# Optimization experiments

Measured on AMD Instinct MI355X. Metric: run time of the kernel, lower is better.

The kernel has to match this reference:

```python
import jax, jax.numpy as jnp
import numpy as np

NUM_EXPERTS = 8
TOP_K = 2
N_EMBD = 1024
B, T = 4, 2048


def setup_inputs() -> dict:
    key = jax.random.key(0)
    k_x, k_g, k_e = jax.random.split(key, 3)
    x = jax.random.normal(k_x, (B, T, N_EMBD), dtype=jnp.float32)
    # torch nn.Linear weight layout: (out_features, in_features); y = x @ W.T
    scale = 1.0 / np.sqrt(N_EMBD)
    gate_w = jax.random.uniform(k_g, (NUM_EXPERTS, N_EMBD), dtype=jnp.float32,
                                minval=-scale, maxval=scale)
    expert_w = jax.random.uniform(k_e, (NUM_EXPERTS, N_EMBD, N_EMBD), dtype=jnp.float32,
                                  minval=-scale, maxval=scale)
    return {"x": x, "gate_w": gate_w, "expert_w": expert_w}


def reference(x, gate_w, expert_w):
    Bb, Tt, C = x.shape
    xf = x.reshape(Bb * Tt, C)                        # (N, C)
    logits = xf @ gate_w.T                            # (N, E)
    w, sel = jax.lax.top_k(logits, TOP_K)             # (N, K) each
    # softmax over the selected logits in float32, cast back (matches torch)
    w = jax.nn.softmax(w.astype(jnp.float32), axis=1).astype(xf.dtype)
    # scatter per-token routing weights into a dense (N, E) combine matrix
    n = xf.shape[0]
    w_full = jnp.zeros((n, NUM_EXPERTS), dtype=xf.dtype)
    w_full = w_full.at[jnp.arange(n)[:, None], sel].add(w)
    # all-expert outputs: y_e = x @ W_e.T  -> (N, E, C)
    expert_out = jnp.einsum('nc,edc->ned', xf, expert_w)
    out = jnp.einsum('ne,ned->nd', w_full, expert_out)  # combine
    return out.reshape(Bb, Tt, C)
```

## Files before the change

### kernel.cpp

```cpp
#include <hip/hip_runtime.h>
#include <hip/hip_bf16.h>

#define NEXP 8
#define NEMB 1024
#define NTOK 8192
#define BM 128
#define BN 256
#define BK 64
#define NK  (NEMB / BK)
#define RBSLOTS 20
#define BLD_STRIPE 512

typedef __attribute__((ext_vector_type(8))) short  bf16x8;
typedef __attribute__((ext_vector_type(8))) unsigned short u16x8;
typedef __attribute__((ext_vector_type(4))) float  f32x4;

#define XB_BYTES   (NTOK * NEMB * 2)
#define WB_BYTES   (NEXP * NEMB * NEMB * 2)
#define CNT_OFF    (XB_BYTES + WB_BYTES)
#define LTOK_OFF   (CNT_OFF + 256)
#define LWT_OFF    (LTOK_OFF + NEXP * NTOK * 4)
#define SELW_OFF   (LWT_OFF + NEXP * NTOK * 4)

__device__ __forceinline__ unsigned short f2bf(float f) {
    unsigned u = __builtin_bit_cast(unsigned, f);
    unsigned r = (u + 0x7fffu + ((u >> 16) & 1u)) >> 16;
    return (unsigned short)r;
}

__global__ void k_cvt_w(const float* __restrict__ w, unsigned short* __restrict__ wb) {
    int i = (blockIdx.x * blockDim.x + threadIdx.x) * 8;
    f32x4 v0 = *reinterpret_cast<const f32x4*>(w + i);
    f32x4 v1 = *reinterpret_cast<const f32x4*>(w + i + 4);
    u16x8 o;
#pragma unroll
    for (int j = 0; j < 4; ++j) { o[j] = f2bf(v0[j]); o[4 + j] = f2bf(v1[j]); }
    *reinterpret_cast<u16x8*>(wb + i) = o;
}

__global__ __launch_bounds__(256)
void k_gate(const float* __restrict__ x, const float* __restrict__ gw,
            unsigned short* __restrict__ xb, int4* __restrict__ selw) {
    int t = threadIdx.x, wave = t >> 6, lane = t & 63;
    int n = blockIdx.x * 4 + wave;

    const float* xr = x + (size_t)n * NEMB + lane * 16;
    f32x4 xv[4];
#pragma unroll
    for (int j = 0; j < 4; ++j) xv[j] = *reinterpret_cast<const f32x4*>(xr + j * 4);

    u16x8 o0, o1;
#pragma unroll
    for (int q = 0; q < 4; ++q) {
        o0[q] = f2bf(xv[0][q]); o0[4 + q] = f2bf(xv[1][q]);
        o1[q] = f2bf(xv[2][q]); o1[4 + q] = f2bf(xv[3][q]);
    }
    u16x8* xo = reinterpret_cast<u16x8*>(xb + (size_t)n * NEMB + lane * 16);
    xo[0] = o0; xo[1] = o1;

    float p[NEXP];
#pragma unroll
    for (int e = 0; e < NEXP; ++e) {
        const float* gr = gw + e * NEMB + lane * 16;
        f32x4 a = xv[0] * *reinterpret_cast<const f32x4*>(gr);
#pragma unroll
        for (int j = 1; j < 4; ++j) a += xv[j] * *reinterpret_cast<const f32x4*>(gr + j * 4);
        p[e] = a[0] + a[1] + a[2] + a[3];
    }
#pragma unroll
    for (int e = 0; e < NEXP; ++e) {
        float v = p[e];
#pragma unroll
        for (int m = 1; m < 64; m <<= 1) v += __shfl_xor(v, m, 64);
        p[e] = v;
    }
    if (lane == 0) {
        int e0 = 0; float b0 = p[0];
#pragma unroll
        for (int e = 1; e < NEXP; ++e) if (p[e] > b0) { b0 = p[e]; e0 = e; }
        int e1 = -1; float b1 = -3.4e38f;
#pragma unroll
        for (int e = 0; e < NEXP; ++e) if (e != e0 && p[e] > b1) { b1 = p[e]; e1 = e; }
        float ex = __expf(b1 - b0);
        float inv = 1.f / (1.f + ex);
        int4 s;
        s.x = e0; s.y = e1;
        s.z = __float_as_int(inv); s.w = __float_as_int(ex * inv);
        selw[n] = s;
    }
}

__global__ __launch_bounds__(256)
void k_build(const int4* __restrict__ selw, int* __restrict__ counts,
             int* __restrict__ ltok, float* __restrict__ lwt) {
    int e = blockIdx.y;
    int n0 = blockIdx.x * BLD_STRIPE;
    __shared__ int lcnt, base;
    __shared__ int   toks[BLD_STRIPE];
    __shared__ float wts[BLD_STRIPE];
    if (threadIdx.x == 0) lcnt = 0;
    __syncthreads();
    for (int i = threadIdx.x; i < BLD_STRIPE; i += 256) {
        int4 s = selw[n0 + i];
        if (s.x == e) {
            int p = atomicAdd(&lcnt, 1);
            toks[p] = n0 + i; wts[p] = __int_as_float(s.z);
        }
        if (s.y == e) {
            int p = atomicAdd(&lcnt, 1);
            toks[p] = n0 + i; wts[p] = __int_as_float(s.w);
        }
    }
    __syncthreads();
    if (threadIdx.x == 0) base = atomicAdd(&counts[e], lcnt);
    __syncthreads();
    for (int i = threadIdx.x; i < lcnt; i += 256) {
        ltok[e * NTOK + base + i] = toks[i];
        lwt[e * NTOK + base + i]  = wts[i];
    }
}

__global__ void k_pad(const int* __restrict__ counts, int* __restrict__ ltok,
                      float* __restrict__ lwt) {
    int e = blockIdx.x;
    int c = counts[e];
    int cp = (c + BM - 1) & ~(BM - 1);
    for (int i = c + threadIdx.x; i < cp; i += blockDim.x) {
        ltok[e * NTOK + i] = -1;
        lwt[e * NTOK + i]  = 0.f;
    }
}

__global__ __launch_bounds__(512, 2)
void k_gemm(const unsigned short* __restrict__ xb, const unsigned short* __restrict__ wb,
            const int* __restrict__ counts, const int* __restrict__ ltok,
            const float* __restrict__ lwt, float* __restrict__ out) {
    int e  = blockIdx.z;
    int rb = blockIdx.y;
    int cb = blockIdx.x;
    int cnt = counts[e];
    if (rb * BM >= cnt) return;

    __shared__ unsigned short As[3][BM * BK];
    __shared__ unsigned short Bs[3][BN * BK];
    __shared__ int   tokS[BM];
    __shared__ float wS[BM];

    int t = threadIdx.x;
    int lane = t & 63, wave = t >> 6;
    int wr = wave >> 2, wc = wave & 3;

    if (t < BM) {
        tokS[t] = ltok[e * NTOK + rb * BM + t];
        wS[t]   = lwt[e * NTOK + rb * BM + t];
    }

    const unsigned short* aSrc[2]; int aOff[2];
    const unsigned short* bSrc[4]; int bOff[4];
#pragma unroll
    for (int i = 0; i < 2; ++i) {
        int idx = i * 512 + t;
        int r   = idx >> 3;
        int csw = (idx & 7) ^ (r & 7);
        int tok = ltok[e * NTOK + rb * BM + r];
        int tokc = tok < 0 ? 0 : tok;
        aSrc[i] = xb + (size_t)tokc * NEMB + csw * 8;
        aOff[i] = (i * 512 + wave * 64) * 8;
    }
#pragma unroll
    for (int i = 0; i < 4; ++i) {
        int idx = i * 512 + t;
        int r   = idx >> 3;
        int csw = (idx & 7) ^ (r & 7);
        bSrc[i] = wb + (size_t)e * NEMB * NEMB + (size_t)(cb * BN + r) * NEMB + csw * 8;
        bOff[i] = (i * 512 + wave * 64) * 8;
    }

#define STAGE(aDst, bDst, kk)                                                       \
    {                                                                               \
        _Pragma("unroll")                                                           \
        for (int i = 0; i < 2; ++i)                                                 \
            __builtin_amdgcn_global_load_lds(                                       \
                (const __attribute__((address_space(1))) void*)(aSrc[i] + (kk) * BK),\
                (__attribute__((address_space(3))) void*)((aDst) + aOff[i]), 16, 0, 0);\
        _Pragma("unroll")                                                           \
        for (int i = 0; i < 4; ++i)                                                 \
            __builtin_amdgcn_global_load_lds(                                       \
                (const __attribute__((address_space(1))) void*)(bSrc[i] + (kk) * BK),\
                (__attribute__((address_space(3))) void*)((bDst) + bOff[i]), 16, 0, 0);\
    }

    f32x4 acc[4][4];
#pragma unroll
    for (int m = 0; m < 4; ++m)
#pragma unroll
        for (int n = 0; n < 4; ++n) acc[m][n] = (f32x4){0.f, 0.f, 0.f, 0.f};

    int fr = lane & 15, fq = lane >> 4, fs = fr & 7;

#define COMPUTE(aRd, bRd)                                                           \
    {                                                                               \
        _Pragma("unroll")                                                           \
        for (int ks = 0; ks < 2; ++ks) {                                            \
            int ch = (fq + 4 * ks) ^ fs;                                            \
            bf16x8 af[4], bfr[4];                                                   \
            _Pragma("unroll")                                                       \
            for (int m = 0; m < 4; ++m)                                             \
                af[m] = *reinterpret_cast<const bf16x8*>(                           \
                    (aRd) + (wr * 64 + m * 16 + fr) * BK + ch * 8);                 \
            _Pragma("unroll")                                                       \
            for (int n = 0; n < 4; ++n)                                             \
                bfr[n] = *reinterpret_cast<const bf16x8*>(                          \
                    (bRd) + (wc * 64 + n * 16 + fr) * BK + ch * 8);                 \
            __builtin_amdgcn_s_setprio(1);                                          \
            _Pragma("unroll")                                                       \
            for (int m = 0; m < 4; ++m)                                             \
                _Pragma("unroll")                                                   \
                for (int n = 0; n < 4; ++n)                                         \
                    acc[m][n] = __builtin_amdgcn_mfma_f32_16x16x32_bf16(            \
                        af[m], bfr[n], acc[m][n], 0, 0, 0);                         \
            __builtin_amdgcn_s_setprio(0);                                          \
        }                                                                           \
    }

    unsigned short *aRd = &As[0][0], *aMid = &As[1][0], *aWr = &As[2][0];
    unsigned short *bRd = &Bs[0][0], *bMid = &Bs[1][0], *bWr = &Bs[2][0];

    STAGE(aRd, bRd, 0);
    STAGE(aMid, bMid, 1);

    for (int kt = 0; kt < NK - 2; ++kt) {
        asm volatile("s_waitcnt vmcnt(6)" ::: "memory");
        __builtin_amdgcn_s_barrier();
        STAGE(aWr, bWr, kt + 2);
        COMPUTE(aRd, bRd);
        asm volatile("s_waitcnt lgkmcnt(0)" ::: "memory");
        __builtin_amdgcn_s_barrier();
        unsigned short* tmp;
        tmp = aRd; aRd = aMid; aMid = aWr; aWr = tmp;
        tmp = bRd; bRd = bMid; bMid = bWr; bWr = tmp;
    }
    asm volatile("s_waitcnt vmcnt(6)" ::: "memory");
    __builtin_amdgcn_s_barrier();
    COMPUTE(aRd, bRd);
    asm volatile("s_waitcnt lgkmcnt(0)" ::: "memory");
    __builtin_amdgcn_s_barrier();
    {
        unsigned short* tmp;
        tmp = aRd; aRd = aMid; aMid = aWr; aWr = tmp;
        tmp = bRd; bRd = bMid; bMid = bWr; bWr = tmp;
    }
    asm volatile("s_waitcnt vmcnt(0)" ::: "memory");
    __builtin_amdgcn_s_barrier();
    COMPUTE(aRd, bRd);
#undef STAGE
#undef COMPUTE

#pragma unroll
    for (int m = 0; m < 4; ++m) {
#pragma unroll
        for (int jj = 0; jj < 4; ++jj) {
            int row = wr * 64 + m * 16 + fq * 4 + jj;
            int tok = tokS[row];
            if (tok < 0) continue;
            float wgt = wS[row];
            float* orow = out + (size_t)tok * NEMB + cb * BN + wc * 64 + fr;
#pragma unroll
            for (int n = 0; n < 4; ++n)
                unsafeAtomicAdd(orow + n * 16, wgt * acc[m][n][jj]);
        }
    }
}

extern "C" void kernel_launch(void* const* d_in, const int* in_sizes, int n_in,
                              void* d_out, int out_size, void* d_ws, size_t ws_size,
                              hipStream_t stream) {
    const float* x  = (const float*)d_in[0];
    const float* gw = (const float*)d_in[1];
    const float* ew = (const float*)d_in[2];
    float* out = (float*)d_out;

    char* ws = (char*)d_ws;
    unsigned short* xb = (unsigned short*)(ws);
    unsigned short* wb = (unsigned short*)(ws + XB_BYTES);
    int*   counts = (int*)(ws + CNT_OFF);
    int*   ltok   = (int*)(ws + LTOK_OFF);
    float* lwt    = (float*)(ws + LWT_OFF);
    int4*  selw   = (int4*)(ws + SELW_OFF);

    hipMemsetAsync(counts, 0, 8 * sizeof(int), stream);
    hipMemsetAsync(out, 0, (size_t)NTOK * NEMB * sizeof(float), stream);

    k_cvt_w<<<4096, 256, 0, stream>>>(ew, wb);
    k_gate<<<NTOK / 4, 256, 0, stream>>>(x, gw, xb, selw);
    k_build<<<dim3(NTOK / BLD_STRIPE, NEXP), 256, 0, stream>>>(selw, counts, ltok, lwt);
    k_pad<<<8, 128, 0, stream>>>(counts, ltok, lwt);
    k_gemm<<<dim3(NEMB / BN, RBSLOTS, NEXP), 512, 0, stream>>>(xb, wb, counts, ltok, lwt, out);
}
```

Baseline: 157.1 us.

## Enlarge M tile to 256 with BK=32 and interleave staged loads with MFMA

Doubles the row tile per block (BM 256) while halving the K step (BK 32), so each wave owns 128x64 outputs and reuses its B fragments across eight M sub-tiles. The main loop is rewritten into a single three-buffer pipeline that issues the A and B global-to-LDS loads at separate points between the two MFMA halves, and drops the trailing barrier per iteration. The aim is higher arithmetic intensity per LDS byte and better overlap of memory with compute. The cost is twice the accumulator registers (lower occupancy), twice as many K iterations with their barriers, and more padded rows per expert at the larger tile.

```diff
diff --git a/kernel.cpp b/kernel.cpp
--- a/kernel.cpp
+++ b/kernel.cpp
@@ -4,11 +4,11 @@
 #define NEXP 8
 #define NEMB 1024
 #define NTOK 8192
-#define BM 128
+#define BM 256
 #define BN 256
-#define BK 64
+#define BK 32
 #define NK  (NEMB / BK)
-#define RBSLOTS 20
+#define RBSLOTS 16
 #define BLD_STRIPE 512
 
 typedef __attribute__((ext_vector_type(8))) short  bf16x8;
@@ -155,112 +155,107 @@
         wS[t]   = lwt[e * NTOK + rb * BM + t];
     }
 
-    const unsigned short* aSrc[2]; int aOff[2];
-    const unsigned short* bSrc[4]; int bOff[4];
+    const unsigned short* aSrc[2];
+    const unsigned short* bSrc[2];
+    int ldOff[2];
 #pragma unroll
     for (int i = 0; i < 2; ++i) {
         int idx = i * 512 + t;
-        int r   = idx >> 3;
-        int csw = (idx & 7) ^ (r & 7);
+        int r   = idx >> 2;
+        int csw = (idx & 3) ^ (r & 3);
         int tok = ltok[e * NTOK + rb * BM + r];
         int tokc = tok < 0 ? 0 : tok;
         aSrc[i] = xb + (size_t)tokc * NEMB + csw * 8;
-        aOff[i] = (i * 512 + wave * 64) * 8;
-    }
-#pragma unroll
-    for (int i = 0; i < 4; ++i) {
-        int idx = i * 512 + t;
-        int r   = idx >> 3;
-        int csw = (idx & 7) ^ (r & 7);
         bSrc[i] = wb + (size_t)e * NEMB * NEMB + (size_t)(cb * BN + r) * NEMB + csw * 8;
-        bOff[i] = (i * 512 + wave * 64) * 8;
-    }
-
-#define STAGE(aDst, bDst, kk)                                                       \
+        ldOff[i] = (i * 512 + wave * 64) * 8;
+    }
+
+#define STAGE_A(dst, kk)                                                            \
     {                                                                               \
         _Pragma("unroll")                                                           \
         for (int i = 0; i < 2; ++i)                                                 \
             __builtin_amdgcn_global_load_lds(                                       \
                 (const __attribute__((address_space(1))) void*)(aSrc[i] + (kk) * BK),\
-                (__attribute__((address_space(3))) void*)((aDst) + aOff[i]), 16, 0, 0);\
+                (__attribute__((address_space(3))) void*)((dst) + ldOff[i]), 16, 0, 0);\
+    }
+#define STAGE_B(dst, kk)                                                            \
+    {                                                                               \
         _Pragma("unroll")                                                           \
-        for (int i = 0; i < 4; ++i)                                                 \
+        for (int i = 0; i < 2; ++i)                                                 \
             __builtin_amdgcn_global_load_lds(                                       \
                 (const __attribute__((address_space(1))) void*)(bSrc[i] + (kk) * BK),\
-                (__attribute__((address_space(3))) void*)((bDst) + bOff[i]), 16, 0, 0);\
-    }
-
-    f32x4 acc[4][4];
-#pragma unroll
-    for (int m = 0; m < 4; ++m)
+                (__attribute__((address_space(3))) void*)((dst) + ldOff[i]), 16, 0, 0);\
+    }
+
+    f32x4 acc[8][4];
+#pragma unroll
+    for (int m = 0; m < 8; ++m)
 #pragma unroll
         for (int n = 0; n < 4; ++n) acc[m][n] = (f32x4){0.f, 0.f, 0.f, 0.f};
 
-    int fr = lane & 15, fq = lane >> 4, fs = fr & 7;
-
-#define COMPUTE(aRd, bRd)                                                           \
-    {                                                                               \
-        _Pragma("unroll")                                                           \
-        for (int ks = 0; ks < 2; ++ks) {                                            \
-            int ch = (fq + 4 * ks) ^ fs;                                            \
-            bf16x8 af[4], bfr[4];                                                   \
-            _Pragma("unroll")                                                       \
-            for (int m = 0; m < 4; ++m)                                             \
-                af[m] = *reinterpret_cast<const bf16x8*>(                           \
-                    (aRd) + (wr * 64 + m * 16 + fr) * BK + ch * 8);                 \
-            _Pragma("unroll")                                                       \
-            for (int n = 0; n < 4; ++n)                                             \
-                bfr[n] = *reinterpret_cast<const bf16x8*>(                          \
-                    (bRd) + (wc * 64 + n * 16 + fr) * BK + ch * 8);                 \
-            __builtin_amdgcn_s_setprio(1);                                          \
-            _Pragma("unroll")                                                       \
-            for (int m = 0; m < 4; ++m)                                             \
-                _Pragma("unroll")                                                   \
-                for (int n = 0; n < 4; ++n)                                         \
-                    acc[m][n] = __builtin_amdgcn_mfma_f32_16x16x32_bf16(            \
-                        af[m], bfr[n], acc[m][n], 0, 0, 0);                         \
-            __builtin_amdgcn_s_setprio(0);                                          \
-        }                                                                           \
-    }
-
-    unsigned short *aRd = &As[0][0], *aMid = &As[1][0], *aWr = &As[2][0];
-    unsigned short *bRd = &Bs[0][0], *bMid = &Bs[1][0], *bWr = &Bs[2][0];
-
-    STAGE(aRd, bRd, 0);
-    STAGE(aMid, bMid, 1);
-
-    for (int kt = 0; kt < NK - 2; ++kt) {
-        asm volatile("s_waitcnt vmcnt(6)" ::: "memory");
+    int fr = lane & 15, fq = lane >> 4;
+    int ch = fq ^ (fr & 3);
+    int aBase = (wr * 128 + fr) * BK + ch * 8;
+    int bBase = (wc * 64  + fr) * BK + ch * 8;
+
+    STAGE_A(&As[0][0], 0); STAGE_B(&Bs[0][0], 0);
+    STAGE_A(&As[1][0], 1); STAGE_B(&Bs[1][0], 1);
+
+    for (int tau = 0; tau < NK; ++tau) {
+        const unsigned short* aCur = &As[tau % 3][0];
+        const unsigned short* bCur = &Bs[tau % 3][0];
+        unsigned short* aNxt = &As[(tau + 2) % 3][0];
+        unsigned short* bNxt = &Bs[(tau + 2) % 3][0];
+
+        if (tau < NK - 1) { asm volatile("s_waitcnt vmcnt(4)" ::: "memory"); }
+        else              { asm volatile("s_waitcnt vmcnt(0)" ::: "memory"); }
+        __builtin_amdgcn_sched_barrier(0);
         __builtin_amdgcn_s_barrier();
-        STAGE(aWr, bWr, kt + 2);
-        COMPUTE(aRd, bRd);
+
+        bool doStage = (tau + 2) < NK;
+
+        if (doStage) STAGE_A(aNxt, tau + 2);
+        bf16x8 bfr[4], af[4];
+#pragma unroll
+        for (int n = 0; n < 4; ++n)
+            bfr[n] = *reinterpret_cast<const bf16x8*>(bCur + bBase + n * 16 * BK);
+#pragma unroll
+        for (int m = 0; m < 4; ++m)
+            af[m] = *reinterpret_cast<const bf16x8*>(aCur + aBase + m * 16 * BK);
         asm volatile("s_waitcnt lgkmcnt(0)" ::: "memory");
-        __builtin_amdgcn_s_barrier();
-        unsigned short* tmp;
-        tmp = aRd; aRd = aMid; aMid = aWr; aWr = tmp;
-        tmp = bRd; bRd = bMid; bMid = bWr; bWr = tmp;
-    }
-    asm volatile("s_waitcnt vmcnt(6)" ::: "memory");
-    __builtin_amdgcn_s_barrier();
-    COMPUTE(aRd, bRd);
-    asm volatile("s_waitcnt lgkmcnt(0)" ::: "memory");
-    __builtin_amdgcn_s_barrier();
-    {
-        unsigned short* tmp;
-        tmp = aRd; aRd = aMid; aMid = aWr; aWr = tmp;
-        tmp = bRd; bRd = bMid; bMid = bWr; bWr = tmp;
-    }
-    asm volatile("s_waitcnt vmcnt(0)" ::: "memory");
-    __builtin_amdgcn_s_barrier();
-    COMPUTE(aRd, bRd);
-#undef STAGE
-#undef COMPUTE
-
-#pragma unroll
-    for (int m = 0; m < 4; ++m) {
+        __builtin_amdgcn_sched_barrier(0);
+        __builtin_amdgcn_s_setprio(1);
+#pragma unroll
+        for (int m = 0; m < 4; ++m)
+#pragma unroll
+            for (int n = 0; n < 4; ++n)
+                acc[m][n] = __builtin_amdgcn_mfma_f32_16x16x32_bf16(
+                    af[m], bfr[n], acc[m][n], 0, 0, 0);
+        __builtin_amdgcn_s_setprio(0);
+
+        if (doStage) STAGE_B(bNxt, tau + 2);
+#pragma unroll
+        for (int m = 0; m < 4; ++m)
+            af[m] = *reinterpret_cast<const bf16x8*>(aCur + aBase + (m + 4) * 16 * BK);
+        asm volatile("s_waitcnt lgkmcnt(0)" ::: "memory");
+        __builtin_amdgcn_sched_barrier(0);
+        __builtin_amdgcn_s_setprio(1);
+#pragma unroll
+        for (int m = 0; m < 4; ++m)
+#pragma unroll
+            for (int n = 0; n < 4; ++n)
+                acc[m + 4][n] = __builtin_amdgcn_mfma_f32_16x16x32_bf16(
+                    af[m], bfr[n], acc[m + 4][n], 0, 0, 0);
+        __builtin_amdgcn_s_setprio(0);
+    }
+#undef STAGE_A
+#undef STAGE_B
+
+#pragma unroll
+    for (int m = 0; m < 8; ++m) {
 #pragma unroll
         for (int jj = 0; jj < 4; ++jj) {
-            int row = wr * 64 + m * 16 + fq * 4 + jj;
+            int row = wr * 128 + m * 16 + fq * 4 + jj;
             int tok = tokS[row];
             if (tok < 0) continue;
             float wgt = wS[row];
```

Result: slower. 160.5 us (+2.2%).
